# Kernel optimization log

Hardware: AMD Instinct MI355X
Metric: run time of the kernel (lower is better)

Reference implementation:

```python
import jax, jax.numpy as jnp
import numpy as np

D = 2048   # embed_dim
E = 128    # expand_ratio = head dim
H = D // E # num heads = 16
C = 64     # chunk size for the chunked linear-attention scan
EPS = 1e-6


def setup_inputs() -> dict:
    key = jax.random.key(0)
    ks = jax.random.split(key, 6)
    b, n = 2, 2048
    s = 0.02
    x = jax.random.normal(ks[0], (b, n, D), jnp.float32)
    Wq = (jax.random.normal(ks[1], (D, D), jnp.float32) * s)
    Wk = (jax.random.normal(ks[2], (D, D), jnp.float32) * s)
    Wv = (jax.random.normal(ks[3], (D, D), jnp.float32) * s)
    Wf = (jax.random.normal(ks[4], (D, H), jnp.float32) * s)
    Wo = (jax.random.normal(ks[5], (D, D), jnp.float32) * s)
    norm_w = jnp.ones((D,), jnp.float32)
    return {"x": x, "Wq": Wq, "Wk": Wk, "Wv": Wv, "Wf": Wf, "Wo": Wo, "norm_w": norm_w}


def _lightning_scalar_decay(q, k, v, ld):
    # q,k,v: [b,n,H,E], ld: [b,n,H] log decay per head per step.
    # Recurrence: S_t = exp(ld_t) * S_{t-1} + k_t^T v_t ; o_t = q_t @ S_t
    b, n, h, e = q.shape
    nc = n // C
    qc = q.reshape(b, nc, C, h, e)
    kc = k.reshape(b, nc, C, h, e)
    vc = v.reshape(b, nc, C, h, e)
    ldc = ld.reshape(b, nc, C, h)
    cum = jnp.cumsum(ldc, axis=2)          # inclusive within-chunk log decay [b,nc,C,h]
    tot = cum[:, :, -1, :]                 # [b,nc,h]

    # intra-chunk: scores[i,j] = (q_i . k_j) * exp(L_i - L_j), j <= i
    Lh = cum.transpose(0, 1, 3, 2)         # [b,nc,h,C]
    decay = jnp.exp(Lh[..., :, None] - Lh[..., None, :])  # [b,nc,h,C,C]
    mask = jnp.tril(jnp.ones((C, C), bool))
    scores = jnp.einsum('bmihe,bmjhe->bmhij', qc, kc) * decay
    scores = jnp.where(mask, scores, 0.0)
    o_intra = jnp.einsum('bmhij,bmjhe->bmihe', scores, vc)

    # inter-chunk: carried recurrent state S [b,h,e,e]
    def step(S, inp):
        q_c, k_c, v_c, cum_c, tot_c = inp  # [b,C,h,e],...,[b,C,h],[b,h]
        o = jnp.einsum('bihe,bhef->bihf', q_c * jnp.exp(cum_c)[..., None], S)
        kd = k_c * jnp.exp(tot_c[:, None, :] - cum_c)[..., None]
        S_new = S * jnp.exp(tot_c)[:, :, None, None] + jnp.einsum('bihe,bihf->bhef', kd, v_c)
        return S_new, o

    xs = (qc.transpose(1, 0, 2, 3, 4), kc.transpose(1, 0, 2, 3, 4),
          vc.transpose(1, 0, 2, 3, 4), cum.transpose(1, 0, 2, 3), tot.transpose(1, 0, 2))
    S0 = jnp.zeros((b, h, e, e), q.dtype)
    S_final, o_inter = jax.lax.scan(step, S0, xs)
    o_inter = o_inter.transpose(1, 0, 2, 3, 4)  # [b,nc,C,h,e]
    return (o_intra + o_inter).reshape(b, n, h * e), S_final


def reference(x, Wq, Wk, Wv, Wf, Wo, norm_w):
    b, n, d = x.shape
    q = jax.nn.silu(x @ Wq).reshape(b, n, H, E)
    k = jax.nn.silu(x @ Wk).reshape(b, n, H, E)
    v = (x @ Wv).reshape(b, n, H, E)
    ld = jax.nn.log_sigmoid(x @ Wf)  # [b,n,H]
    o, _ = _lightning_scalar_decay(q, k, v, ld)
    # RMSNorm over full embed dim
    o = o * jax.lax.rsqrt(jnp.mean(o * o, axis=-1, keepdims=True) + EPS) * norm_w
    return o @ Wo
```

## Files before the change

### kernel.cpp

```cpp
#include <hip/hip_runtime.h>
#include <hip/hip_bf16.h>
#include <stdint.h>

#define D_ 2048
#define E_ 128
#define H_ 16
#define NB_ 2
#define NSEQ_ 2048
#define NTOK_ 4096
#define NCH_ 32

typedef short bf16s;
typedef __attribute__((ext_vector_type(8))) short bf16x8;
typedef __attribute__((ext_vector_type(4))) float f32x4;

__device__ __forceinline__ short f2b(float f) {
  __hip_bfloat16 h = __float2bfloat16(f);
  return *reinterpret_cast<short*>(&h);
}
__device__ __forceinline__ float b2f(short s) {
  __hip_bfloat16 h;
  *reinterpret_cast<short*>(&h) = s;
  return __bfloat162float(h);
}

__device__ __forceinline__ void gload_lds16(const void* g, void* l) {
  __builtin_amdgcn_global_load_lds(
      (__attribute__((address_space(1))) void*)(const_cast<void*>(g)),
      (__attribute__((address_space(3))) void*)(l), 16, 0, 0);
}

__device__ __forceinline__ void barrier_mem() {
  asm volatile("s_barrier" ::: "memory");
}
template <int N>
__device__ __forceinline__ void wait_vmcnt() {
  if constexpr (N == 0) asm volatile("s_waitcnt vmcnt(0)" ::: "memory");
  else if constexpr (N == 1) asm volatile("s_waitcnt vmcnt(1)" ::: "memory");
  else asm volatile("s_waitcnt vmcnt(2)" ::: "memory");
}

__global__ __launch_bounds__(256)
void cvt_bf16(const float* __restrict__ x, bf16s* __restrict__ y) {
  const size_t i = (size_t)blockIdx.x * 256 + threadIdx.x;
  const float4 a = ((const float4*)x)[i * 2];
  const float4 b = ((const float4*)x)[i * 2 + 1];
  bf16x8 o;
  o[0] = f2b(a.x); o[1] = f2b(a.y); o[2] = f2b(a.z); o[3] = f2b(a.w);
  o[4] = f2b(b.x); o[5] = f2b(b.y); o[6] = f2b(b.z); o[7] = f2b(b.w);
  *(bf16x8*)&y[i * 8] = o;
}

__global__ __launch_bounds__(256)
void transpose_w(const float* __restrict__ Wq, const float* __restrict__ Wk,
                 const float* __restrict__ Wv, const float* __restrict__ Wo,
                 bf16s* __restrict__ WqT, bf16s* __restrict__ WkT,
                 bf16s* __restrict__ WvT, bf16s* __restrict__ WoT) {
  const float* src; bf16s* dst;
  if (blockIdx.z == 0)      { src = Wq; dst = WqT; }
  else if (blockIdx.z == 1) { src = Wk; dst = WkT; }
  else if (blockIdx.z == 2) { src = Wv; dst = WvT; }
  else                      { src = Wo; dst = WoT; }
  __shared__ float tile[64][65];
  const int n0 = blockIdx.x * 64, k0 = blockIdx.y * 64;
  const int t = threadIdx.x;
  const int tr = t >> 6, tc = t & 63;
#pragma unroll
  for (int rr = 0; rr < 16; ++rr) {
    const int row = rr * 4 + tr;
    tile[row][tc] = src[(size_t)(k0 + row) * D_ + n0 + tc];
  }
  __syncthreads();
#pragma unroll
  for (int rr = 0; rr < 16; ++rr) {
    const int row = rr * 4 + tr;
    dst[(size_t)(n0 + row) * D_ + k0 + tc] = f2b(tile[tc][row]);
  }
}

__global__ __launch_bounds__(256)
void ld_gemm(const float* __restrict__ x, const float* __restrict__ Wf,
             float* __restrict__ ldb) {
  const int t = threadIdx.x;
  const int col = t & 15;
  const int tok = blockIdx.x * 16 + (t >> 4);
  const float4* xr = (const float4*)(x + (size_t)tok * D_);
  float s = 0.f;
#pragma unroll 4
  for (int kk = 0; kk < D_ / 4; ++kk) {
    const float4 xv = xr[kk];
    const int k4 = kk * 4;
    s += xv.x * Wf[(k4 + 0) * H_ + col];
    s += xv.y * Wf[(k4 + 1) * H_ + col];
    s += xv.z * Wf[(k4 + 2) * H_ + col];
    s += xv.w * Wf[(k4 + 3) * H_ + col];
  }
  const float m = fminf(s, 0.f);
  ldb[(size_t)tok * H_ + col] = m - log1pf(__expf(-fabsf(s)));
}

template <int BN, typename OT>
__device__ __forceinline__ void gemm8p_body(const bf16s* __restrict__ A,
                                            const bf16s* __restrict__ Bt,
                                            OT* __restrict__ C, int bm, int bn,
                                            int act) {
  constexpr int BM = 256, BK = 64;
  constexpr int KT = D_ / BK;
  constexpr int RA = BM / 64;
  constexpr int RB = BN / 64;
  constexpr int RT = RA + RB;
  constexpr int NF = BN / 64;
  __shared__ bf16s As[2][BM * BK];
  __shared__ bf16s Bs[2][BN * BK];

  const int t = threadIdx.x;
  const int w = t >> 6, l = t & 63;
  const int wm = w >> 2, wn = w & 3;
  const int lr = l & 15, lk = l >> 4;
  const int lrow8 = l >> 3, lc = l & 7;
  const int csrc = lc ^ lrow8;

  f32x4 acc[8][NF] = {};

  const size_t arow = (size_t)bm * BM;
  const size_t brow = (size_t)bn * BN;

  auto stage_round = [&](int r, int buf, int k0) {
    if (r < RA) {
      const int row0 = r * 64 + w * 8;
      gload_lds16(&A[(arow + row0 + lrow8) * D_ + k0 + csrc * 8],
                  &As[buf][row0 * BK]);
    } else {
      const int row0 = (r - RA) * 64 + w * 8;
      gload_lds16(&Bt[(brow + row0 + lrow8) * D_ + k0 + csrc * 8],
                  &Bs[buf][row0 * BK]);
    }
  };
  auto lda = [&](int buf, int fm, int ks) -> bf16x8 {
    const int row = wm * 128 + fm * 16 + lr;
    const int cc = (ks * 4 + lk) ^ (row & 7);
    return *(const bf16x8*)&As[buf][row * BK + cc * 8];
  };
  auto ldb_ = [&](int buf, int fn, int ks) -> bf16x8 {
    const int row = wn * (NF * 16) + fn * 16 + lr;
    const int cc = (ks * 4 + lk) ^ (row & 7);
    return *(const bf16x8*)&Bs[buf][row * BK + cc * 8];
  };

#pragma unroll
  for (int r = 0; r < RT; ++r) stage_round(r, 0, 0);

  bf16x8 bfr[NF][2];
  for (int tki = 0; tki < KT - 1; ++tki) {
    const int cur = tki & 1, nxt = cur ^ 1;
    const int k0n = (tki + 1) * BK;
#pragma unroll
    for (int qd = 0; qd < 4; ++qd) {
      const int r0 = (qd * RT) / 4, r1 = ((qd + 1) * RT) / 4;
      if (qd == 0) {
#pragma unroll
        for (int r = r0; r < r1; ++r) stage_round(r, nxt, k0n);
        wait_vmcnt<RT / 4>();
        barrier_mem();
#pragma unroll
        for (int fn = 0; fn < NF; ++fn)
#pragma unroll
          for (int ks = 0; ks < 2; ++ks) bfr[fn][ks] = ldb_(cur, fn, ks);
      }
      bf16x8 af[2][2];
#pragma unroll
      for (int f2 = 0; f2 < 2; ++f2)
#pragma unroll
        for (int ks = 0; ks < 2; ++ks) af[f2][ks] = lda(cur, qd * 2 + f2, ks);
      if (qd != 0) {
#pragma unroll
        for (int r = r0; r < r1; ++r) stage_round(r, nxt, k0n);
        barrier_mem();
      }
      __builtin_amdgcn_s_setprio(1);
#pragma unroll
      for (int f2 = 0; f2 < 2; ++f2)
#pragma unroll
        for (int fn = 0; fn < NF; ++fn)
#pragma unroll
          for (int ks = 0; ks < 2; ++ks)
            acc[qd * 2 + f2][fn] = __builtin_amdgcn_mfma_f32_16x16x32_bf16(
                af[f2][ks], bfr[fn][ks], acc[qd * 2 + f2][fn], 0, 0, 0);
      __builtin_amdgcn_s_setprio(0);
      barrier_mem();
    }
  }
  {
    const int cur = (KT - 1) & 1;
    wait_vmcnt<0>();
    barrier_mem();
#pragma unroll
    for (int fn = 0; fn < NF; ++fn)
#pragma unroll
      for (int ks = 0; ks < 2; ++ks) bfr[fn][ks] = ldb_(cur, fn, ks);
#pragma unroll
    for (int qd = 0; qd < 4; ++qd) {
      bf16x8 af[2][2];
#pragma unroll
      for (int f2 = 0; f2 < 2; ++f2)
#pragma unroll
        for (int ks = 0; ks < 2; ++ks) af[f2][ks] = lda(cur, qd * 2 + f2, ks);
#pragma unroll
      for (int f2 = 0; f2 < 2; ++f2)
#pragma unroll
        for (int fn = 0; fn < NF; ++fn)
#pragma unroll
          for (int ks = 0; ks < 2; ++ks)
            acc[qd * 2 + f2][fn] = __builtin_amdgcn_mfma_f32_16x16x32_bf16(
                af[f2][ks], bfr[fn][ks], acc[qd * 2 + f2][fn], 0, 0, 0);
    }
  }
#pragma unroll
  for (int fm = 0; fm < 8; ++fm) {
    const int row = bm * BM + wm * 128 + fm * 16 + lk * 4;
#pragma unroll
    for (int fn = 0; fn < NF; ++fn) {
      const int col = bn * BN + wn * (NF * 16) + fn * 16 + lr;
#pragma unroll
      for (int r = 0; r < 4; ++r) {
        float vv = acc[fm][fn][r];
        if (act) vv = vv / (1.f + __expf(-vv));
        if constexpr (sizeof(OT) == 2)
          C[(size_t)(row + r) * D_ + col] = f2b(vv);
        else
          C[(size_t)(row + r) * D_ + col] = vv;
      }
    }
  }
}

__global__ __launch_bounds__(512, 2)
void gemm_qkv8(const bf16s* __restrict__ xb, const bf16s* __restrict__ WqT,
               const bf16s* __restrict__ WkT, const bf16s* __restrict__ WvT,
               bf16s* __restrict__ qb, bf16s* __restrict__ kb,
               bf16s* __restrict__ vb) {
  const int bn = blockIdx.x, bm = blockIdx.y;
  const int im = bn >> 3, bnl = bn & 7;
  const bf16s* Bt = (im == 0) ? WqT : (im == 1 ? WkT : WvT);
  bf16s* out = (im == 0) ? qb : (im == 1 ? kb : vb);
  gemm8p_body<256, bf16s>(xb, Bt, out, bm, bnl, im < 2);
}

__global__ __launch_bounds__(512, 2)
void gemm_out8(const bf16s* __restrict__ ob, const bf16s* __restrict__ WoT,
               float* __restrict__ out) {
  gemm8p_body<128, float>(ob, WoT, out, blockIdx.y, blockIdx.x, 0);
}

__global__ __launch_bounds__(256)
void chunk_state(const bf16s* __restrict__ k, const bf16s* __restrict__ v,
                 const float* __restrict__ ldp, bf16s* __restrict__ Mbuf,
                 float* __restrict__ totb) {
  const int c = blockIdx.x, bh = blockIdx.y;
  const int b = bh >> 4, h = bh & 15;
  const int t = threadIdx.x;
  const int w = t >> 6, l = t & 63;
  const int lr = l & 15, lk = l >> 4;

  __shared__ bf16s Kt[64 * 128];
  __shared__ bf16s Vn[64 * 128];
  __shared__ bf16s KdT[128 * 64];
  __shared__ bf16s VtT[128 * 64];
  __shared__ float cumS[64];
  char* cKt = (char*)Kt; char* cVn = (char*)Vn;
  char* cKdT = (char*)KdT; char* cVtT = (char*)VtT;

  const size_t grow0 = (size_t)b * NSEQ_ + c * 64;
#pragma unroll
  for (int j = 0; j < 4; ++j) {
    const int lrow = w * 16 + j * 4 + (l >> 4);
    const int ck = (l & 15) ^ (lrow & 7);
    const size_t goff = (grow0 + lrow) * D_ + h * E_ + ck * 8;
    const int lbase = (w * 16 + j * 4) * 128;
    gload_lds16(&k[goff], &Kt[lbase]);
    gload_lds16(&v[goff], &Vn[lbase]);
  }
  if (w == 0) {
    float val = ldp[(grow0 + l) * H_ + h];
#pragma unroll
    for (int off = 1; off < 64; off <<= 1) {
      float pv = __shfl_up(val, off);
      if (l >= off) val += pv;
    }
    cumS[l] = val;
  }
  __syncthreads();
  const float tot = cumS[63];
  if (t == 0) totb[bh * NCH_ + c] = tot;

#pragma unroll
  for (int it = 0; it < 4; ++it) {
    const int task = t + it * 256;
    const int i = task >> 4, cx = task & 15;
    const int sb = i * 256 + ((cx * 16) ^ ((i & 7) << 4));
    bf16x8 vv = *(const bf16x8*)(cVn + sb);
    bf16x8 kk8 = *(const bf16x8*)(cKt + sb);
    const float sE = __expf(tot - cumS[i]);
#pragma unroll
    for (int jj = 0; jj < 8; ++jj) {
      const int e = cx * 8 + jj;
      const int db = e * 128 + ((i * 2) ^ ((e & 7) << 4));
      *(bf16s*)(cVtT + db) = vv[jj];
      *(bf16s*)(cKdT + db) = f2b(b2f(kk8[jj]) * sE);
    }
  }
  __syncthreads();

  const int wm = w >> 1, wn = w & 1;
  f32x4 acc[4][4] = {};
#pragma unroll
  for (int kk2 = 0; kk2 < 2; ++kk2) {
    const int cb = (kk2 * 32 + lk * 8) * 2;
    bf16x8 af[4], bfr[4];
#pragma unroll
    for (int tm = 0; tm < 4; ++tm) {
      const int fr = wm * 64 + tm * 16 + lr;
      af[tm] = *(const bf16x8*)(cVtT + fr * 128 + (cb ^ ((fr & 7) << 4)));
    }
#pragma unroll
    for (int tn = 0; tn < 4; ++tn) {
      const int er = wn * 64 + tn * 16 + lr;
      bfr[tn] = *(const bf16x8*)(cKdT + er * 128 + (cb ^ ((er & 7) << 4)));
    }
#pragma unroll
    for (int tm = 0; tm < 4; ++tm)
#pragma unroll
      for (int tn = 0; tn < 4; ++tn)
        acc[tm][tn] = __builtin_amdgcn_mfma_f32_16x16x32_bf16(
            af[tm], bfr[tn], acc[tm][tn], 0, 0, 0);
  }
  const size_t mb = (size_t)(bh * NCH_ + c) * 128 * 128;
#pragma unroll
  for (int tm = 0; tm < 4; ++tm) {
#pragma unroll
    for (int tn = 0; tn < 4; ++tn) {
#pragma unroll
      for (int r = 0; r < 4; ++r) {
        const int f = wm * 64 + tm * 16 + lk * 4 + r;
        const int e = wn * 64 + tn * 16 + lr;
        Mbuf[mb + f * 128 + e] = f2b(acc[tm][tn][r]);
      }
    }
  }
}

__global__ __launch_bounds__(256)
void state_scan(const bf16s* __restrict__ Mbuf, const float* __restrict__ totb,
                bf16s* __restrict__ Sbuf) {
  const int sl = blockIdx.x;
  const int bh = blockIdx.y;
  const int t = threadIdx.x;
  const int fr = sl * 16 + (t >> 4);
  const int e0 = (t & 15) * 8;
  const size_t base = ((size_t)(bh * NCH_) * 128 + fr) * 128 + e0;
  const size_t cstride = 128 * 128;
  float acc[8] = {};
  bf16x8 m = *(const bf16x8*)&Mbuf[base];
  for (int c = 0; c < NCH_; ++c) {
    bf16x8 sv;
#pragma unroll
    for (int j = 0; j < 8; ++j) sv[j] = f2b(acc[j]);
    *(bf16x8*)&Sbuf[base + (size_t)c * cstride] = sv;
    bf16x8 mn = m;
    if (c + 1 < NCH_) mn = *(const bf16x8*)&Mbuf[base + (size_t)(c + 1) * cstride];
    const float dt = __expf(totb[bh * NCH_ + c]);
#pragma unroll
    for (int j = 0; j < 8; ++j) acc[j] = acc[j] * dt + b2f(m[j]);
    m = mn;
  }
}

__global__ __launch_bounds__(256)
void attn_out(const bf16s* __restrict__ q, const bf16s* __restrict__ k,
              const bf16s* __restrict__ v, const float* __restrict__ ldp,
              const bf16s* __restrict__ Sbuf, bf16s* __restrict__ o) {
  const int c = blockIdx.x, bh = blockIdx.y;
  const int b = bh >> 4, h = bh & 15;
  const int t = threadIdx.x;
  const int w = t >> 6, l = t & 63;
  const int lr = l & 15, lk = l >> 4;

  __shared__ bf16s Qt[64 * 128];
  __shared__ bf16s Kt[64 * 128];
  __shared__ bf16s Vn[64 * 128];
  __shared__ bf16s VtT[128 * 64];
  __shared__ bf16s St[128 * 128];
  __shared__ bf16s Pm[64 * 64];
  __shared__ float cumS[64];
  char* cQt = (char*)Qt; char* cKt = (char*)Kt; char* cVn = (char*)Vn;
  char* cVtT = (char*)VtT; char* cSt = (char*)St; char* cPm = (char*)Pm;

  const size_t grow0 = (size_t)b * NSEQ_ + c * 64;
  const size_t sbase = (size_t)(bh * NCH_ + c) * 128 * 128;
#pragma unroll
  for (int j = 0; j < 4; ++j) {
    const int lrow = w * 16 + j * 4 + (l >> 4);
    const int ck = (l & 15) ^ (lrow & 7);
    const size_t goff = (grow0 + lrow) * D_ + h * E_ + ck * 8;
    const int lbase = (w * 16 + j * 4) * 128;
    gload_lds16(&q[goff], &Qt[lbase]);
    gload_lds16(&k[goff], &Kt[lbase]);
    gload_lds16(&v[goff], &Vn[lbase]);
  }
#pragma unroll
  for (int j = 0; j < 8; ++j) {
    const int lrow = w * 32 + j * 4 + (l >> 4);
    const int ck = (l & 15) ^ (lrow & 7);
    gload_lds16(&Sbuf[sbase + (size_t)lrow * 128 + ck * 8],
                &St[(w * 32 + j * 4) * 128]);
  }
  if (w == 0) {
    float val = ldp[(grow0 + l) * H_ + h];
#pragma unroll
    for (int off = 1; off < 64; off <<= 1) {
      float pv = __shfl_up(val, off);
      if (l >= off) val += pv;
    }
    cumS[l] = val;
  }
  __syncthreads();

#pragma unroll
  for (int it = 0; it < 4; ++it) {
    const int task = t + it * 256;
    const int i = task >> 4, cx = task & 15;
    const int sb = i * 256 + ((cx * 16) ^ ((i & 7) << 4));
    bf16x8 vv = *(const bf16x8*)(cVn + sb);
#pragma unroll
    for (int jj = 0; jj < 8; ++jj) {
      const int e = cx * 8 + jj;
      const int db = e * 128 + ((i * 2) ^ ((e & 7) << 4));
      *(bf16s*)(cVtT + db) = vv[jj];
    }
  }

  f32x4 accs[4] = {};
  f32x4 acco[8] = {};
#pragma unroll
  for (int kk = 0; kk < 4; ++kk) {
    const int cb = (kk * 32 + lk * 8) * 2;
    const int ar = w * 16 + lr;
    bf16x8 aq = *(const bf16x8*)(cQt + ar * 256 + (cb ^ ((ar & 7) << 4)));
#pragma unroll
    for (int tn = 0; tn < 4; ++tn) {
      const int br = tn * 16 + lr;
      bf16x8 bk = *(const bf16x8*)(cKt + br * 256 + (cb ^ ((br & 7) << 4)));
      accs[tn] = __builtin_amdgcn_mfma_f32_16x16x32_bf16(aq, bk, accs[tn], 0, 0, 0);
    }
#pragma unroll
    for (int tf = 0; tf < 8; ++tf) {
      const int sr = tf * 16 + lr;
      bf16x8 bs = *(const bf16x8*)(cSt + sr * 256 + (cb ^ ((sr & 7) << 4)));
      acco[tf] = __builtin_amdgcn_mfma_f32_16x16x32_bf16(aq, bs, acco[tf], 0, 0, 0);
    }
  }
#pragma unroll
  for (int r = 0; r < 4; ++r) {
    const float gI = __expf(cumS[w * 16 + lk * 4 + r]);
#pragma unroll
    for (int tf = 0; tf < 8; ++tf) acco[tf][r] *= gI;
  }
#pragma unroll
  for (int tn = 0; tn < 4; ++tn) {
    const int j = tn * 16 + lr;
    const float cj = cumS[j];
#pragma unroll
    for (int r = 0; r < 4; ++r) {
      const int i = w * 16 + lk * 4 + r;
      const float sv = (j <= i) ? accs[tn][r] * __expf(cumS[i] - cj) : 0.f;
      *(bf16s*)(cPm + i * 128 + ((j * 2) ^ ((i & 7) << 4))) = f2b(sv);
    }
  }
  __syncthreads();

#pragma unroll
  for (int kk2 = 0; kk2 < 2; ++kk2) {
    const int cb = (kk2 * 32 + lk * 8) * 2;
    const int pr = w * 16 + lr;
    bf16x8 ap = *(const bf16x8*)(cPm + pr * 128 + (cb ^ ((pr & 7) << 4)));
#pragma unroll
    for (int tf = 0; tf < 8; ++tf) {
      const int fr = tf * 16 + lr;
      bf16x8 bv = *(const bf16x8*)(cVtT + fr * 128 + (cb ^ ((fr & 7) << 4)));
      acco[tf] = __builtin_amdgcn_mfma_f32_16x16x32_bf16(ap, bv, acco[tf], 0, 0, 0);
    }
  }
#pragma unroll
  for (int tf = 0; tf < 8; ++tf) {
#pragma unroll
    for (int r = 0; r < 4; ++r) {
      const int i = w * 16 + lk * 4 + r;
      o[(grow0 + i) * D_ + h * E_ + tf * 16 + lr] = f2b(acco[tf][r]);
    }
  }
}

__global__ __launch_bounds__(256)
void rmsnorm(bf16s* __restrict__ o, const float* __restrict__ nw) {
  const int tok = blockIdx.x;
  const int t = threadIdx.x;
  bf16s* row = o + (size_t)tok * D_;
  bf16x8 vv = *(bf16x8*)&row[t * 8];
  float f[8];
  float s = 0.f;
#pragma unroll
  for (int j = 0; j < 8; ++j) { f[j] = b2f(vv[j]); s += f[j] * f[j]; }
#pragma unroll
  for (int off2 = 32; off2 > 0; off2 >>= 1) s += __shfl_down(s, off2);
  __shared__ float wsum[4];
  if ((t & 63) == 0) wsum[t >> 6] = s;
  __syncthreads();
  const float scale =
      rsqrtf((wsum[0] + wsum[1] + wsum[2] + wsum[3]) * (1.f / D_) + 1e-6f);
  bf16x8 ov;
#pragma unroll
  for (int j = 0; j < 8; ++j) ov[j] = f2b(f[j] * scale * nw[t * 8 + j]);
  *(bf16x8*)&row[t * 8] = ov;
}

extern "C" void kernel_launch(void* const* d_in, const int* in_sizes, int n_in,
                              void* d_out, int out_size, void* d_ws,
                              size_t ws_size, hipStream_t stream) {
  (void)in_sizes; (void)n_in; (void)out_size;
  const float* x  = (const float*)d_in[0];
  const float* Wq = (const float*)d_in[1];
  const float* Wk = (const float*)d_in[2];
  const float* Wv = (const float*)d_in[3];
  const float* Wf = (const float*)d_in[4];
  const float* Wo = (const float*)d_in[5];
  const float* nw = (const float*)d_in[6];
  float* out = (float*)d_out;

  char* ws = (char*)d_ws;
  const size_t MB = 1024 * 1024;
  bf16s* xb   = (bf16s*)(ws + 0);
  bf16s* WqT  = (bf16s*)(ws + 16 * MB);
  bf16s* WkT  = (bf16s*)(ws + 24 * MB);
  bf16s* WvT  = (bf16s*)(ws + 32 * MB);
  bf16s* Sbuf = (bf16s*)(ws + 0);
  float* totb = (float*)(ws + 32 * MB);
  bf16s* WoT  = (bf16s*)(ws + 40 * MB);
  bf16s* qb   = (bf16s*)(ws + 48 * MB);
  bf16s* kb   = (bf16s*)(ws + 64 * MB);
  bf16s* vb   = (bf16s*)(ws + 80 * MB);
  bf16s* ob   = (bf16s*)(ws + 96 * MB);
  bf16s* Mbuf = (bf16s*)(ws + 112 * MB);
  float* ldb  = (float*)(ws + 144 * MB);
  if (145 * MB > ws_size) return;

  cvt_bf16<<<NTOK_ * D_ / 8 / 256, 256, 0, stream>>>(x, xb);
  transpose_w<<<dim3(32, 32, 4), 256, 0, stream>>>(Wq, Wk, Wv, Wo, WqT, WkT,
                                                   WvT, WoT);
  ld_gemm<<<NTOK_ / 16, 256, 0, stream>>>(x, Wf, ldb);
  gemm_qkv8<<<dim3(24, 16), 512, 0, stream>>>(xb, WqT, WkT, WvT, qb, kb, vb);
  chunk_state<<<dim3(NCH_, NB_ * H_), 256, 0, stream>>>(kb, vb, ldb, Mbuf, totb);
  state_scan<<<dim3(8, NB_ * H_), 256, 0, stream>>>(Mbuf, totb, Sbuf);
  attn_out<<<dim3(NCH_, NB_ * H_), 256, 0, stream>>>(qb, kb, vb, ldb, Sbuf, ob);
  rmsnorm<<<NTOK_, 256, 0, stream>>>(ob, nw);
  gemm_out8<<<dim3(16, 16), 512, 0, stream>>>(ob, WoT, out);
}
```

Before: 341.9 us.

## Rework GEMM mainloop into 4-slot BK=32 prefetch pipeline with 3 stages in flight

Replaces the double-buffered BK=64 GEMM mainloop, which interleaved staging across quarter-steps, with a 4-slot ring of BK=32 tiles. Three stages are kept in flight and vmcnt waits allow the outstanding loads. The LDS swizzle changes to match the 32-wide rows, and each step does one barrier-guarded compute over all fragments. The aim is to hide global load latency better, at the cost of twice as many barriers per K and less MFMA work between syncs. LDS use stays the same.

```diff
diff --git a/kernel.cpp b/kernel.cpp
--- a/kernel.cpp
+++ b/kernel.cpp
@@ -35,9 +35,14 @@
 }
 template <int N>
 __device__ __forceinline__ void wait_vmcnt() {
-  if constexpr (N == 0) asm volatile("s_waitcnt vmcnt(0)" ::: "memory");
-  else if constexpr (N == 1) asm volatile("s_waitcnt vmcnt(1)" ::: "memory");
-  else asm volatile("s_waitcnt vmcnt(2)" ::: "memory");
+  if constexpr (N == 0)       asm volatile("s_waitcnt vmcnt(0)" ::: "memory");
+  else if constexpr (N == 3)  asm volatile("s_waitcnt vmcnt(3)" ::: "memory");
+  else if constexpr (N == 4)  asm volatile("s_waitcnt vmcnt(4)" ::: "memory");
+  else if constexpr (N == 6)  asm volatile("s_waitcnt vmcnt(6)" ::: "memory");
+  else if constexpr (N == 8)  asm volatile("s_waitcnt vmcnt(8)" ::: "memory");
+  else if constexpr (N == 9)  asm volatile("s_waitcnt vmcnt(9)" ::: "memory");
+  else if constexpr (N == 12) asm volatile("s_waitcnt vmcnt(12)" ::: "memory");
+  else static_assert(N == 0, "unsupported vmcnt");
 }
 
 __global__ __launch_bounds__(256)
@@ -100,121 +105,86 @@
 }
 
 template <int BN, typename OT>
-__device__ __forceinline__ void gemm8p_body(const bf16s* __restrict__ A,
-                                            const bf16s* __restrict__ Bt,
-                                            OT* __restrict__ C, int bm, int bn,
-                                            int act) {
-  constexpr int BM = 256, BK = 64;
+__device__ __forceinline__ void gemm_dp_body(const bf16s* __restrict__ A,
+                                             const bf16s* __restrict__ Bt,
+                                             OT* __restrict__ C, int bm, int bn,
+                                             int act) {
+  constexpr int BM = 256, BK = 32;
   constexpr int KT = D_ / BK;
-  constexpr int RA = BM / 64;
-  constexpr int RB = BN / 64;
-  constexpr int RT = RA + RB;
   constexpr int NF = BN / 64;
-  __shared__ bf16s As[2][BM * BK];
-  __shared__ bf16s Bs[2][BN * BK];
+  constexpr int SLOT_A = BM * BK;
+  constexpr int SLOT_B = BN * BK;
+  constexpr int LPS = 2 + BN / 128;
+  __shared__ bf16s As[4 * SLOT_A];
+  __shared__ bf16s Bs[4 * SLOT_B];
 
   const int t = threadIdx.x;
   const int w = t >> 6, l = t & 63;
   const int wm = w >> 2, wn = w & 3;
   const int lr = l & 15, lk = l >> 4;
-  const int lrow8 = l >> 3, lc = l & 7;
-  const int csrc = lc ^ lrow8;
+  const int srow = w * 16 + (l >> 2);
+  const int sc = l & 3;
 
   f32x4 acc[8][NF] = {};
-
   const size_t arow = (size_t)bm * BM;
   const size_t brow = (size_t)bn * BN;
 
-  auto stage_round = [&](int r, int buf, int k0) {
-    if (r < RA) {
-      const int row0 = r * 64 + w * 8;
-      gload_lds16(&A[(arow + row0 + lrow8) * D_ + k0 + csrc * 8],
-                  &As[buf][row0 * BK]);
-    } else {
-      const int row0 = (r - RA) * 64 + w * 8;
-      gload_lds16(&Bt[(brow + row0 + lrow8) * D_ + k0 + csrc * 8],
-                  &Bs[buf][row0 * BK]);
+  auto stage = [&](int s) {
+    const int slot = s & 3;
+    const int k0 = s * BK;
+#pragma unroll
+    for (int r = 0; r < 2; ++r) {
+      const int row = r * 128 + srow;
+      const int cs = sc ^ ((row >> 1) & 3);
+      gload_lds16(&A[(arow + row) * D_ + k0 + cs * 8],
+                  &As[slot * SLOT_A + (r * 128 + w * 16) * BK]);
+    }
+#pragma unroll
+    for (int r = 0; r < BN / 128; ++r) {
+      const int row = r * 128 + srow;
+      const int cs = sc ^ ((row >> 1) & 3);
+      gload_lds16(&Bt[(brow + row) * D_ + k0 + cs * 8],
+                  &Bs[slot * SLOT_B + (r * 128 + w * 16) * BK]);
     }
   };
-  auto lda = [&](int buf, int fm, int ks) -> bf16x8 {
-    const int row = wm * 128 + fm * 16 + lr;
-    const int cc = (ks * 4 + lk) ^ (row & 7);
-    return *(const bf16x8*)&As[buf][row * BK + cc * 8];
+
+  auto compute = [&](int s) {
+    const int slot = s & 3;
+    bf16x8 af[8], bfr[NF];
+#pragma unroll
+    for (int fm = 0; fm < 8; ++fm) {
+      const int row = wm * 128 + fm * 16 + lr;
+      af[fm] = *(const bf16x8*)
+          &As[slot * SLOT_A + row * BK + (lk ^ ((row >> 1) & 3)) * 8];
+    }
+#pragma unroll
+    for (int fn = 0; fn < NF; ++fn) {
+      const int row = wn * (NF * 16) + fn * 16 + lr;
+      bfr[fn] = *(const bf16x8*)
+          &Bs[slot * SLOT_B + row * BK + (lk ^ ((row >> 1) & 3)) * 8];
+    }
+    __builtin_amdgcn_s_setprio(1);
+#pragma unroll
+    for (int fm = 0; fm < 8; ++fm)
+#pragma unroll
+      for (int fn = 0; fn < NF; ++fn)
+        acc[fm][fn] = __builtin_amdgcn_mfma_f32_16x16x32_bf16(
+            af[fm], bfr[fn], acc[fm][fn], 0, 0, 0);
+    __builtin_amdgcn_s_setprio(0);
   };
-  auto ldb_ = [&](int buf, int fn, int ks) -> bf16x8 {
-    const int row = wn * (NF * 16) + fn * 16 + lr;
-    const int cc = (ks * 4 + lk) ^ (row & 7);
-    return *(const bf16x8*)&Bs[buf][row * BK + cc * 8];
-  };
-
-#pragma unroll
-  for (int r = 0; r < RT; ++r) stage_round(r, 0, 0);
-
-  bf16x8 bfr[NF][2];
-  for (int tki = 0; tki < KT - 1; ++tki) {
-    const int cur = tki & 1, nxt = cur ^ 1;
-    const int k0n = (tki + 1) * BK;
-#pragma unroll
-    for (int qd = 0; qd < 4; ++qd) {
-      const int r0 = (qd * RT) / 4, r1 = ((qd + 1) * RT) / 4;
-      if (qd == 0) {
-#pragma unroll
-        for (int r = r0; r < r1; ++r) stage_round(r, nxt, k0n);
-        wait_vmcnt<RT / 4>();
-        barrier_mem();
-#pragma unroll
-        for (int fn = 0; fn < NF; ++fn)
-#pragma unroll
-          for (int ks = 0; ks < 2; ++ks) bfr[fn][ks] = ldb_(cur, fn, ks);
-      }
-      bf16x8 af[2][2];
-#pragma unroll
-      for (int f2 = 0; f2 < 2; ++f2)
-#pragma unroll
-        for (int ks = 0; ks < 2; ++ks) af[f2][ks] = lda(cur, qd * 2 + f2, ks);
-      if (qd != 0) {
-#pragma unroll
-        for (int r = r0; r < r1; ++r) stage_round(r, nxt, k0n);
-        barrier_mem();
-      }
-      __builtin_amdgcn_s_setprio(1);
-#pragma unroll
-      for (int f2 = 0; f2 < 2; ++f2)
-#pragma unroll
-        for (int fn = 0; fn < NF; ++fn)
-#pragma unroll
-          for (int ks = 0; ks < 2; ++ks)
-            acc[qd * 2 + f2][fn] = __builtin_amdgcn_mfma_f32_16x16x32_bf16(
-                af[f2][ks], bfr[fn][ks], acc[qd * 2 + f2][fn], 0, 0, 0);
-      __builtin_amdgcn_s_setprio(0);
-      barrier_mem();
-    }
-  }
-  {
-    const int cur = (KT - 1) & 1;
-    wait_vmcnt<0>();
+
+  stage(0); stage(1); stage(2);
+  for (int s = 0; s < KT - 3; ++s) {
+    stage(s + 3);
+    wait_vmcnt<3 * LPS>();
     barrier_mem();
-#pragma unroll
-    for (int fn = 0; fn < NF; ++fn)
-#pragma unroll
-      for (int ks = 0; ks < 2; ++ks) bfr[fn][ks] = ldb_(cur, fn, ks);
-#pragma unroll
-    for (int qd = 0; qd < 4; ++qd) {
-      bf16x8 af[2][2];
-#pragma unroll
-      for (int f2 = 0; f2 < 2; ++f2)
-#pragma unroll
-        for (int ks = 0; ks < 2; ++ks) af[f2][ks] = lda(cur, qd * 2 + f2, ks);
-#pragma unroll
-      for (int f2 = 0; f2 < 2; ++f2)
-#pragma unroll
-        for (int fn = 0; fn < NF; ++fn)
-#pragma unroll
-          for (int ks = 0; ks < 2; ++ks)
-            acc[qd * 2 + f2][fn] = __builtin_amdgcn_mfma_f32_16x16x32_bf16(
-                af[f2][ks], bfr[fn][ks], acc[qd * 2 + f2][fn], 0, 0, 0);
-    }
-  }
+    compute(s);
+    barrier_mem();
+  }
+  wait_vmcnt<2 * LPS>(); barrier_mem(); compute(KT - 3); barrier_mem();
+  wait_vmcnt<LPS>();     barrier_mem(); compute(KT - 2); barrier_mem();
+  wait_vmcnt<0>();       barrier_mem(); compute(KT - 1);
+
 #pragma unroll
   for (int fm = 0; fm < 8; ++fm) {
     const int row = bm * BM + wm * 128 + fm * 16 + lk * 4;
@@ -243,13 +213,13 @@
   const int im = bn >> 3, bnl = bn & 7;
   const bf16s* Bt = (im == 0) ? WqT : (im == 1 ? WkT : WvT);
   bf16s* out = (im == 0) ? qb : (im == 1 ? kb : vb);
-  gemm8p_body<256, bf16s>(xb, Bt, out, bm, bnl, im < 2);
+  gemm_dp_body<256, bf16s>(xb, Bt, out, bm, bnl, im < 2);
 }
 
 __global__ __launch_bounds__(512, 2)
 void gemm_out8(const bf16s* __restrict__ ob, const bf16s* __restrict__ WoT,
                float* __restrict__ out) {
-  gemm8p_body<128, float>(ob, WoT, out, blockIdx.y, blockIdx.x, 0);
+  gemm_dp_body<128, float>(ob, WoT, out, blockIdx.y, blockIdx.x, 0);
 }
 
 __global__ __launch_bounds__(256)
```

Result: slower. 369.9 us (+8.2%).
